# Kernel optimization log

Measured on AMD Instinct MI355X. Metric: run time of the kernel, lower is better.

## Reference

```python
import jax, jax.numpy as jnp
import numpy as np

B, N, D = 32768, 50, 128  # batch, neighbours, embedding_dim


def setup_inputs() -> dict:
    key = jax.random.key(0)
    k1, k2, k3, k4 = jax.random.split(key, 4)
    scale = 1.0 / np.sqrt(D)
    return {
        "mainNodeEmbed": jax.random.normal(k1, (B, D), dtype=jnp.float32),
        "neighbourNodesEmbeds": jax.random.normal(k2, (B, N, D), dtype=jnp.float32),
        "W": jax.random.normal(k3, (D, D), dtype=jnp.float32) * scale,            # self.w kernel (no bias)
        "A_w": jax.random.normal(k4, (2 * D, D), dtype=jnp.float32) * scale,      # attentionDense kernel
        "A_b": jnp.zeros((D,), dtype=jnp.float32),                                 # attentionDense bias
    }


def reference(mainNodeEmbed, neighbourNodesEmbeds, W, A_w, A_b):
    # Linear projections (shared weight, no bias)
    px = mainNodeEmbed @ W                       # [B, D]
    pn = neighbourNodesEmbeds @ W                # [B, N, D]
    # mode == 'repeat': tile main node across neighbours, concat on feature dim
    px_rep = jnp.broadcast_to(px[:, None, :], pn.shape)   # [B, N, D]
    cat = jnp.concatenate([px_rep, pn], axis=2)           # [B, N, 2D]
    # attention logits: Dense + leaky_relu (tf default alpha=0.2)
    e_ij = jax.nn.leaky_relu(cat @ A_w + A_b, negative_slope=0.2)  # [B, N, D]
    # softmax over the neighbour axis (axis=1), per feature channel
    a_ij = jax.nn.softmax(e_ij, axis=1)
    # attention-weighted sum over neighbours
    return jnp.sum(a_ij * pn, axis=1)            # [B, D]
```

## Files before the change

### kernel.cpp

```cpp
#include <hip/hip_runtime.h>
#include <math.h>

#define NN 50
#define DD 128
#define MT 4
#define KT 4
#define NIT 64
#define ROWS 51
#define TILE_B (ROWS * 512)
#define NBUF 3

typedef __attribute__((ext_vector_type(4))) float  f32x4;
typedef __attribute__((ext_vector_type(2))) __fp16 f16x2;
typedef __attribute__((ext_vector_type(8))) __fp16 f16x8;

__device__ float g_WA1f[DD * DD];
__device__ float g_WA2f[DD * DD];
__device__ __attribute__((aligned(16))) __fp16 g_Wt[3 * DD * DD];

__global__ void compute_WA(const float* __restrict__ W,
                           const float* __restrict__ A_w) {
    const int d = threadIdx.x, k = blockIdx.x, m = blockIdx.y;
    const float* __restrict__ A = A_w + (size_t)m * DD * DD;
    float acc = 0.f;
#pragma unroll 8
    for (int j = 0; j < DD; ++j)
        acc = fmaf(W[k * DD + j], A[j * DD + d], acc);
    if (m == 0) g_WA1f[k * DD + d] = acc;
    else        g_WA2f[k * DD + d] = acc;
}

__global__ void cvt_weights(const float* __restrict__ W) {
    const int n = blockIdx.x;
    const int k = threadIdx.x;
    float v;
    if (n < DD)          v = W[k * DD + n];
    else if (n < 2 * DD) v = g_WA2f[k * DD + (n - DD)];
    else                 v = g_WA1f[k * DD + (n - 2 * DD)];
    g_Wt[n * DD + k] = (__fp16)v;
}

__device__ __forceinline__ f16x8 cvt8(float4 f0, float4 f1) {
    union { f16x2 h[4]; f16x8 v; } u;
    u.h[0] = __builtin_amdgcn_cvt_pkrtz(f0.x, f0.y);
    u.h[1] = __builtin_amdgcn_cvt_pkrtz(f0.z, f0.w);
    u.h[2] = __builtin_amdgcn_cvt_pkrtz(f1.x, f1.y);
    u.h[3] = __builtin_amdgcn_cvt_pkrtz(f1.z, f1.w);
    return u.v;
}

#define MFMA(a, b, c) __builtin_amdgcn_mfma_f32_16x16x32_f16((a), (b), (c), 0, 0, 0)

__global__ __launch_bounds__(256, 2)
void attn_mfma(const float* __restrict__ x,
               const float* __restrict__ nbr,
               const float* __restrict__ A_b,
               float* __restrict__ out, int B) {
    __shared__ __attribute__((aligned(16))) char tiles[NBUF][TILE_B];
    __shared__ __attribute__((aligned(16))) char dummy_lds[64];

    const int tid  = threadIdx.x;
    const int w    = tid >> 6;
    const int lane = tid & 63;
    const int c    = lane & 15;
    const int g    = lane >> 4;
    const size_t b0 = (size_t)blockIdx.x * NIT;

    f16x8 bF[3][2][KT];
#pragma unroll
    for (int p = 0; p < 3; ++p)
#pragma unroll
        for (int nt = 0; nt < 2; ++nt)
#pragma unroll
            for (int kt = 0; kt < KT; ++kt) {
                const int col = p * DD + 32 * w + 16 * nt + c;
                bF[p][nt][kt] = *reinterpret_cast<const f16x8*>(
                    g_Wt + col * DD + 32 * kt + 8 * g);
                asm volatile("" : "+v"(bF[p][nt][kt]));
            }
    float ab0 = A_b[32 * w + c];
    float ab1 = A_b[32 * w + 16 + c];
    asm volatile("" : "+v"(ab0), "+v"(ab1));

    auto stage = [&](int it, char* dst) {
        const size_t bidx = b0 + (size_t)(it < 0 ? 0 : it);
        const char* nb = (const char*)(nbr + bidx * (NN * DD));
        const char* xb = (const char*)(x + bidx * DD);
#pragma unroll
        for (int j = 0; j < 7; ++j) {
            const int p = w + 4 * j;
            if (it >= 0 && p < 25) {
                const int dloc = p * 1024 + lane * 16;
                const int row  = dloc >> 9;
                const int src  = dloc ^ ((row & 7) << 4);
                __builtin_amdgcn_global_load_lds(
                    (const __attribute__((address_space(1))) void*)(nb + src),
                    (__attribute__((address_space(3))) void*)(dst + p * 1024),
                    16, 0, 0);
            } else if (it >= 0 && p == 25) {
                if (lane < 32) {
                    const int src = (lane * 16) ^ ((50 & 7) << 4);
                    __builtin_amdgcn_global_load_lds(
                        (const __attribute__((address_space(1))) void*)(xb + src),
                        (__attribute__((address_space(3))) void*)(dst + 50 * 512),
                        16, 0, 0);
                }
            } else {
                __builtin_amdgcn_global_load_lds(
                    (const __attribute__((address_space(1))) void*)x,
                    (__attribute__((address_space(3))) void*)dummy_lds, 4, 0, 0);
            }
        }
    };

    char* bufA = tiles[0];
    char* bufB = tiles[1];
    char* bufC = tiles[2];

    stage(0, bufA);
    stage(1, bufB);
#pragma unroll
    for (int j = 0; j < 4; ++j)
        __builtin_amdgcn_global_load_lds(
            (const __attribute__((address_space(1))) void*)x,
            (__attribute__((address_space(3))) void*)dummy_lds, 4, 0, 0);

    const float m0v = (g == 0) ? 1.f : 0.f;

#pragma unroll 1
    for (int i = 0; i < NIT; ++i) {
        const int t2 = i + 2;
        stage(t2 < NIT ? t2 : -1, bufC);

        asm volatile("s_waitcnt vmcnt(18)" ::: "memory");
        __builtin_amdgcn_s_barrier();

        const char* __restrict__ tile = bufA;
        f32x4 acc[MT][2][2];
        f32x4 acc2[2];
#pragma unroll
        for (int mt = 0; mt < MT; ++mt)
#pragma unroll
            for (int p = 0; p < 2; ++p)
#pragma unroll
                for (int nt = 0; nt < 2; ++nt) acc[mt][p][nt] = (f32x4)0.f;
        acc2[0] = (f32x4)0.f; acc2[1] = (f32x4)0.f;

#pragma unroll
        for (int mt = 0; mt < MT; ++mt) {
            int row = 16 * mt + c;
            if (row > 50) row = 50;
            const int rb = row * 512;
            const int sw = (row & 7) << 4;
            f16x8 afr[KT];
#pragma unroll
            for (int kt = 0; kt < KT; ++kt) {
                const int off = rb + kt * 128 + g * 32;
                const float4 lo = *(const float4*)(tile + ((off) ^ sw));
                const float4 hi = *(const float4*)(tile + ((off + 16) ^ sw));
                afr[kt] = cvt8(lo, hi);
            }
#pragma unroll
            for (int kt = 0; kt < KT; ++kt)
#pragma unroll
                for (int p = 0; p < 2; ++p)
#pragma unroll
                    for (int nt = 0; nt < 2; ++nt)
                        acc[mt][p][nt] = MFMA(afr[kt], bF[p][nt][kt], acc[mt][p][nt]);
            if (mt == 3) {
#pragma unroll
                for (int kt = 0; kt < KT; ++kt)
#pragma unroll
                    for (int nt = 0; nt < 2; ++nt)
                        acc2[nt] = MFMA(afr[kt], bF[2][nt][kt], acc2[nt]);
            }
        }

#pragma unroll
        for (int nt = 0; nt < 2; ++nt) {
            const float pxa = __shfl(acc2[nt][2], c) + (nt ? ab1 : ab0);
            float den = 0.f, num = 0.f;
#pragma unroll
            for (int mt = 0; mt < MT; ++mt)
#pragma unroll
                for (int r = 0; r < 4; ++r) {
                    if (mt == 3 && r >= 2) continue;
                    float t = pxa + acc[mt][1][nt][r];
                    t = fmaxf(t, 0.2f * t);
                    float p = __expf(t);
                    if (mt == 3) p *= m0v;
                    den += p;
                    num = fmaf(p, acc[mt][0][nt][r], num);
                }
            den += __shfl_xor(den, 16); den += __shfl_xor(den, 32);
            num += __shfl_xor(num, 16); num += __shfl_xor(num, 32);
            if (g == 0) out[(b0 + i) * DD + 32 * w + 16 * nt + c] =
                __fdividef(num, den);
        }

        asm volatile("s_waitcnt lgkmcnt(0)" ::: "memory");
        __builtin_amdgcn_sched_barrier(0);
        __builtin_amdgcn_s_barrier();

        char* t0 = bufA; bufA = bufB; bufB = bufC; bufC = t0;
    }
}

extern "C" void kernel_launch(void* const* d_in, const int* in_sizes, int n_in,
                              void* d_out, int out_size, void* d_ws, size_t ws_size,
                              hipStream_t stream) {
    const float* x   = (const float*)d_in[0];
    const float* nbr = (const float*)d_in[1];
    const float* W   = (const float*)d_in[2];
    const float* A_w = (const float*)d_in[3];
    const float* A_b = (const float*)d_in[4];
    float* out = (float*)d_out;
    const int B = in_sizes[0] / DD;

    compute_WA<<<dim3(DD, 2), DD, 0, stream>>>(W, A_w);
    cvt_weights<<<3 * DD, DD, 0, stream>>>(W);
    const int grid = (B + NIT - 1) / NIT;
    attn_mfma<<<grid, 256, 0, stream>>>(x, nbr, A_b, out, B);
}
```

Measured before the change: 252.6 us.

## Stage tiles through registers as fp16 in LDS with double buffering

Replaces the triple-buffered direct global-to-LDS fp32 copies with register-staged loads that are converted to fp16 before being written to LDS. Tiles shrink to half size, so a two-buffer scheme is used, and the A-fragments are read from LDS as single 16-byte f16x8 loads with no per-iteration conversion. The aim is to cut LDS footprint and read bandwidth and to remove conversion work from the MFMA path. In exchange it costs more VGPRs for the in-flight prefetch registers and gives up the asynchronous LDS-DMA path, which may reduce how well memory latency is hidden.

Result: faster. 219.2 us (-13.2%).

```diff
diff --git a/kernel.cpp b/kernel.cpp
--- a/kernel.cpp
+++ b/kernel.cpp
@@ -6,12 +6,11 @@
 #define MT 4
 #define KT 4
 #define NIT 64
-#define ROWS 51
-#define TILE_B (ROWS * 512)
-#define NBUF 3
+#define TILE_H 13056
 
 typedef __attribute__((ext_vector_type(4))) float  f32x4;
 typedef __attribute__((ext_vector_type(2))) __fp16 f16x2;
+typedef __attribute__((ext_vector_type(4))) __fp16 f16x4;
 typedef __attribute__((ext_vector_type(8))) __fp16 f16x8;
 
 __device__ float g_WA1f[DD * DD];
@@ -40,15 +39,6 @@
     g_Wt[n * DD + k] = (__fp16)v;
 }
 
-__device__ __forceinline__ f16x8 cvt8(float4 f0, float4 f1) {
-    union { f16x2 h[4]; f16x8 v; } u;
-    u.h[0] = __builtin_amdgcn_cvt_pkrtz(f0.x, f0.y);
-    u.h[1] = __builtin_amdgcn_cvt_pkrtz(f0.z, f0.w);
-    u.h[2] = __builtin_amdgcn_cvt_pkrtz(f1.x, f1.y);
-    u.h[3] = __builtin_amdgcn_cvt_pkrtz(f1.z, f1.w);
-    return u.v;
-}
-
 #define MFMA(a, b, c) __builtin_amdgcn_mfma_f32_16x16x32_f16((a), (b), (c), 0, 0, 0)
 
 __global__ __launch_bounds__(256, 2)
@@ -56,8 +46,7 @@
                const float* __restrict__ nbr,
                const float* __restrict__ A_b,
                float* __restrict__ out, int B) {
-    __shared__ __attribute__((aligned(16))) char tiles[NBUF][TILE_B];
-    __shared__ __attribute__((aligned(16))) char dummy_lds[64];
+    __shared__ __attribute__((aligned(16))) char tiles[2][TILE_H];
 
     const int tid  = threadIdx.x;
     const int w    = tid >> 6;
@@ -82,60 +71,62 @@
     float ab1 = A_b[32 * w + 16 + c];
     asm volatile("" : "+v"(ab0), "+v"(ab1));
 
-    auto stage = [&](int it, char* dst) {
-        const size_t bidx = b0 + (size_t)(it < 0 ? 0 : it);
-        const char* nb = (const char*)(nbr + bidx * (NN * DD));
-        const char* xb = (const char*)(x + bidx * DD);
+    float4 ra[7];
+    float2 rx;
+
+    auto load_tile = [&](int it) {
+        int itc = it < NIT ? it : NIT - 1;
+        size_t bidx = b0 + (size_t)itc;
+        if (bidx > (size_t)(B - 1)) bidx = (size_t)(B - 1);
+        const float4* __restrict__ nb4 =
+            reinterpret_cast<const float4*>(nbr + bidx * (size_t)(NN * DD));
 #pragma unroll
         for (int j = 0; j < 7; ++j) {
             const int p = w + 4 * j;
-            if (it >= 0 && p < 25) {
-                const int dloc = p * 1024 + lane * 16;
-                const int row  = dloc >> 9;
-                const int src  = dloc ^ ((row & 7) << 4);
-                __builtin_amdgcn_global_load_lds(
-                    (const __attribute__((address_space(1))) void*)(nb + src),
-                    (__attribute__((address_space(3))) void*)(dst + p * 1024),
-                    16, 0, 0);
-            } else if (it >= 0 && p == 25) {
-                if (lane < 32) {
-                    const int src = (lane * 16) ^ ((50 & 7) << 4);
-                    __builtin_amdgcn_global_load_lds(
-                        (const __attribute__((address_space(1))) void*)(xb + src),
-                        (__attribute__((address_space(3))) void*)(dst + 50 * 512),
-                        16, 0, 0);
-                }
-            } else {
-                __builtin_amdgcn_global_load_lds(
-                    (const __attribute__((address_space(1))) void*)x,
-                    (__attribute__((address_space(3))) void*)dummy_lds, 4, 0, 0);
+            if (p < 25) ra[j] = nb4[p * 64 + lane];
+        }
+        if (w == 1)
+            rx = reinterpret_cast<const float2*>(x + bidx * DD)[lane];
+    };
+
+    auto write_tile = [&](char* dst) {
+#pragma unroll
+        for (int j = 0; j < 7; ++j) {
+            const int p = w + 4 * j;
+            if (p < 25) {
+                const int lb  = p * 512 + lane * 8;
+                const int row = lb >> 8;
+                const int ad  = lb ^ ((row & 7) << 4);
+                union { f16x2 h[2]; f16x4 v; } u;
+                u.h[0] = __builtin_amdgcn_cvt_pkrtz(ra[j].x, ra[j].y);
+                u.h[1] = __builtin_amdgcn_cvt_pkrtz(ra[j].z, ra[j].w);
+                *reinterpret_cast<f16x4*>(dst + ad) = u.v;
             }
         }
+        if (w == 1) {
+            const int lb = 50 * 256 + lane * 4;
+            const int ad = lb ^ ((50 & 7) << 4);
+            *reinterpret_cast<f16x2*>(dst + ad) =
+                __builtin_amdgcn_cvt_pkrtz(rx.x, rx.y);
+        }
     };
 
-    char* bufA = tiles[0];
-    char* bufB = tiles[1];
-    char* bufC = tiles[2];
-
-    stage(0, bufA);
-    stage(1, bufB);
-#pragma unroll
-    for (int j = 0; j < 4; ++j)
-        __builtin_amdgcn_global_load_lds(
-            (const __attribute__((address_space(1))) void*)x,
-            (__attribute__((address_space(3))) void*)dummy_lds, 4, 0, 0);
+    load_tile(0);
+    write_tile(tiles[0]);
+    load_tile(1);
+    asm volatile("s_waitcnt lgkmcnt(0)" ::: "memory");
+    __builtin_amdgcn_sched_barrier(0);
+    __builtin_amdgcn_s_barrier();
 
     const float m0v = (g == 0) ? 1.f : 0.f;
 
 #pragma unroll 1
     for (int i = 0; i < NIT; ++i) {
-        const int t2 = i + 2;
-        stage(t2 < NIT ? t2 : -1, bufC);
-
-        asm volatile("s_waitcnt vmcnt(18)" ::: "memory");
-        __builtin_amdgcn_s_barrier();
-
-        const char* __restrict__ tile = bufA;
+        write_tile(tiles[(i + 1) & 1]);
+        load_tile(i + 2);
+        __builtin_amdgcn_sched_barrier(0);
+
+        const char* __restrict__ tile = tiles[i & 1];
         f32x4 acc[MT][2][2];
         f32x4 acc2[2];
 #pragma unroll
@@ -150,16 +141,13 @@
         for (int mt = 0; mt < MT; ++mt) {
             int row = 16 * mt + c;
             if (row > 50) row = 50;
-            const int rb = row * 512;
+            const int rb = row * 256;
             const int sw = (row & 7) << 4;
             f16x8 afr[KT];
 #pragma unroll
-            for (int kt = 0; kt < KT; ++kt) {
-                const int off = rb + kt * 128 + g * 32;
-                const float4 lo = *(const float4*)(tile + ((off) ^ sw));
-                const float4 hi = *(const float4*)(tile + ((off + 16) ^ sw));
-                afr[kt] = cvt8(lo, hi);
-            }
+            for (int kt = 0; kt < KT; ++kt)
+                afr[kt] = *reinterpret_cast<const f16x8*>(
+                    tile + ((rb + kt * 64 + g * 16) ^ sw));
 #pragma unroll
             for (int kt = 0; kt < KT; ++kt)
 #pragma unroll
@@ -201,8 +189,6 @@
         asm volatile("s_waitcnt lgkmcnt(0)" ::: "memory");
         __builtin_amdgcn_sched_barrier(0);
         __builtin_amdgcn_s_barrier();
-
-        char* t0 = bufA; bufA = bufB; bufB = bufC; bufC = t0;
     }
 }
 
```
